# Performance work log

Measured on AMD Instinct MI355X. Metric: run time of the kernel, lower is better.

## Reference

```python
import jax, jax.numpy as jnp
import numpy as np
import math

EPS = 1e-5
K = 4        # conv kernel size
N = 16       # d_state


def setup_inputs() -> dict:
    key = jax.random.key(0)
    b, l, d = 1, 2048, 1024
    di = 2 * d                      # inner channels after split
    dt_rank = math.ceil(d / 16)     # 64
    ks = jax.random.split(key, 8)
    s = 0.02
    return {
        "x": jax.random.normal(ks[0], (b, l, d), jnp.float32),
        "norm_scale": jnp.ones((d,), jnp.float32),
        "w_in": jax.random.normal(ks[1], (d, 4 * d), jnp.float32) * s,
        "conv_w": jax.random.normal(ks[2], (K, 1, di), jnp.float32) * 0.2,
        "conv_b": jnp.zeros((di,), jnp.float32),
        "A_log": jax.random.normal(ks[3], (di, N), jnp.float32) * 0.5,
        "D": jax.random.normal(ks[4], (di,), jnp.float32) * 0.1,
        "w_xproj": jax.random.normal(ks[5], (di, dt_rank + 2 * N), jnp.float32) * s,
        "w_dt": jax.random.normal(ks[6], (dt_rank, di), jnp.float32) * s,
        "b_dt": jnp.zeros((di,), jnp.float32),
        "w_out": jax.random.normal(ks[7], (di, d), jnp.float32) * s,
    }


def _causal_depthwise_conv(x, w, b):
    # x: (b,l,c), w: (K,1,c). Original pads (K-1,K-1) then slices [:, :l] == causal left-pad.
    c = x.shape[-1]
    y = jax.lax.conv_general_dilated(
        x, w, window_strides=(1,), padding=[(K - 1, 0)],
        dimension_numbers=("NWC", "WIO", "NWC"), feature_group_count=c)
    return y + b


def reference(x, norm_scale, w_in, conv_w, conv_b, A_log, D, w_xproj, w_dt, b_dt, w_out):
    dt_rank = w_dt.shape[0]
    # RMSNorm (mean=False, bias=False), scale only
    h = x * jax.lax.rsqrt(jnp.mean(x * x, axis=-1, keepdims=True) + EPS) * norm_scale
    h = h @ w_in                         # (b,l,4d)
    xs, res = jnp.split(h, 2, axis=-1)   # each (b,l,2d)
    res = jax.nn.silu(res)
    xs = jax.nn.silu(_causal_depthwise_conv(xs, conv_w, conv_b))
    proj = xs @ w_xproj                  # (b,l,dt_rank+2N)
    delta, B, C = jnp.split(proj, [dt_rank, dt_rank + N], axis=-1)
    delta = jax.nn.softplus(delta @ w_dt + b_dt)          # (b,l,c)
    A = -jnp.exp(A_log)                                   # (c,n)
    deltaA = jnp.exp(delta[..., None] * A)                # (b,l,c,n)
    deltaBx = (delta * xs)[..., None] * B[:, :, None, :]  # (b,l,c,n)

    def combine(e_i, e_j):
        a_i, b_i = e_i
        a_j, b_j = e_j
        return (a_i * a_j, a_j * b_i + b_j)

    _, ys = jax.lax.associative_scan(combine, (deltaA, deltaBx), axis=1)
    y = jnp.einsum("blcn,bln->blc", ys, C)
    out = (y + xs * D) * res
    return x + out @ w_out
```

## Files before the change

kernel.cpp:

```cpp
#include <hip/hip_runtime.h>

typedef short short8 __attribute__((ext_vector_type(8)));
typedef float floatx4 __attribute__((ext_vector_type(4)));
typedef unsigned int u32;

__device__ __forceinline__ float b2f(unsigned short u) {
    union { unsigned int i; float f; } v; v.i = ((unsigned int)u) << 16; return v.f;
}
__device__ __forceinline__ float hi2f(u32 p) {
    union { unsigned int i; float f; } v; v.i = p & 0xFFFF0000u; return v.f;
}
__device__ __forceinline__ float lo2f(u32 p) {
    union { unsigned int i; float f; } v; v.i = p << 16; return v.f;
}
__device__ __forceinline__ unsigned short f2b(float f) {
    union { unsigned int i; float f; } v; v.f = f;
    unsigned int r = v.i + 0x7FFFu + ((v.i >> 16) & 1u);
    return (unsigned short)(r >> 16);
}
__device__ __forceinline__ float ld(const void* p, size_t i, int f) {
    return f ? ((const float*)p)[i] : b2f(((const unsigned short*)p)[i]);
}
__device__ __forceinline__ void ld4(const void* p, size_t i, int f, float* o) {
    if (f) {
        float4 v = *(const float4*)((const float*)p + i);
        o[0] = v.x; o[1] = v.y; o[2] = v.z; o[3] = v.w;
    } else {
        uint2 v = *(const uint2*)((const unsigned short*)p + i);
        const unsigned short* vp = (const unsigned short*)&v;
        o[0] = b2f(vp[0]); o[1] = b2f(vp[1]); o[2] = b2f(vp[2]); o[3] = b2f(vp[3]);
    }
}
__device__ __forceinline__ int dtf(const void* scale) {
    return (((const unsigned short*)scale)[0] == 0x3F80u) ? 0 : 1;
}
__device__ __forceinline__ void gload16(const unsigned short* g, unsigned short* l) {
    __builtin_amdgcn_global_load_lds(
        (const __attribute__((address_space(1))) u32*)(const void*)g,
        (__attribute__((address_space(3))) u32*)(void*)l, 16, 0, 0);
}
template<int CTRL>
__device__ __forceinline__ float dpp_add(float y) {
    union { float f; int i; } u, r;
    u.f = y;
    r.i = __builtin_amdgcn_update_dpp(0, u.i, CTRL, 0xF, 0xF, true);
    return y + r.f;
}

__global__ __launch_bounds__(256) void prep_kernel(
    const void* x, const void* scale, unsigned short* __restrict__ h,
    const void* w_in, unsigned short* __restrict__ wT,
    const void* w_out, unsigned short* __restrict__ woT)
{
    const int f = dtf(scale);
    const int b = blockIdx.x, tid = threadIdx.x;
    if (b < 2048) {
        const int t = b, i0 = tid * 4;
        float xv[4], sv[4];
        ld4(x, (size_t)t * 1024 + i0, f, xv);
        ld4(scale, (size_t)i0, f, sv);
        float ss = xv[0] * xv[0] + xv[1] * xv[1] + xv[2] * xv[2] + xv[3] * xv[3];
        #pragma unroll
        for (int o = 32; o > 0; o >>= 1) ss += __shfl_down(ss, o);
        __shared__ float sr[4];
        if ((tid & 63) == 0) sr[tid >> 6] = ss;
        __syncthreads();
        float r = rsqrtf((sr[0] + sr[1] + sr[2] + sr[3]) * (1.f / 1024.f) + 1e-5f);
        unsigned short o4[4];
        #pragma unroll
        for (int j = 0; j < 4; j++) o4[j] = f2b(xv[j] * r * sv[j]);
        *(uint2*)(h + (size_t)t * 1024 + i0) = *(const uint2*)o4;
    } else if (b < 3072) {
        __shared__ __align__(8) unsigned short tile[64][72];
        const int idx = b - 2048;
        const int n0 = (idx & 63) * 64, k0 = (idx >> 6) * 64;
        const int r = tid >> 2, cb = (tid & 3) * 16;
        #pragma unroll
        for (int j = 0; j < 4; j++) {
            int c = cb + j * 4;
            float v[4]; unsigned short o4[4];
            ld4(w_in, (size_t)(k0 + r) * 4096 + n0 + c, f, v);
            o4[0] = f2b(v[0]); o4[1] = f2b(v[1]); o4[2] = f2b(v[2]); o4[3] = f2b(v[3]);
            *(uint2*)&tile[r][c] = *(const uint2*)o4;
        }
        __syncthreads();
        #pragma unroll
        for (int j = 0; j < 4; j++) {
            int k = cb + j * 4;
            unsigned short o4[4];
            o4[0] = tile[k][r]; o4[1] = tile[k + 1][r];
            o4[2] = tile[k + 2][r]; o4[3] = tile[k + 3][r];
            *(uint2*)(wT + (size_t)(n0 + r) * 1024 + k0 + k) = *(const uint2*)o4;
        }
    } else {
        __shared__ __align__(8) unsigned short tile[64][72];
        const int idx = b - 3072;
        const int n0 = (idx & 15) * 64, k0 = (idx >> 4) * 64;
        const int r = tid >> 2, cb = (tid & 3) * 16;
        #pragma unroll
        for (int j = 0; j < 4; j++) {
            int c = cb + j * 4;
            float v[4]; unsigned short o4[4];
            ld4(w_out, (size_t)(k0 + r) * 1024 + n0 + c, f, v);
            o4[0] = f2b(v[0]); o4[1] = f2b(v[1]); o4[2] = f2b(v[2]); o4[3] = f2b(v[3]);
            *(uint2*)&tile[r][c] = *(const uint2*)o4;
        }
        __syncthreads();
        #pragma unroll
        for (int j = 0; j < 4; j++) {
            int k = cb + j * 4;
            unsigned short o4[4];
            o4[0] = tile[k][r]; o4[1] = tile[k + 1][r];
            o4[2] = tile[k + 2][r]; o4[3] = tile[k + 3][r];
            *(uint2*)(woT + (size_t)(n0 + r) * 2048 + k0 + k) = *(const uint2*)o4;
        }
    }
}

template<int KDIM, int NDIM, int TM, int TN, int MODE, int XW>
__global__ __launch_bounds__(256) void gemm_bt_kernel(
    const unsigned short* __restrict__ A, const unsigned short* __restrict__ BT,
    void* out0, unsigned short* out1, const void* xres, const void* nscale)
{
    constexpr int RT = TM / 32;
    constexpr int NT = TN / 32;
    constexpr int GX = NDIM / TN, GY = 2048 / TM;
    constexpr int SW = GX / XW, SH = GY / (8 / XW);
    const int f = dtf(nscale);
    __shared__ __align__(16) unsigned short As[TM * 64];
    __shared__ __align__(16) unsigned short Bs[TN * 64];
    const int t = threadIdx.x, w = t >> 6, lane = t & 63;
    const int q = lane >> 4, low = lane & 15;
    const int bid = blockIdx.y * GX + blockIdx.x;
    const int xcd = bid & 7, cc = bid >> 3;
    const int bx = (xcd % XW) * SW + cc % SW;
    const int by = (xcd / XW) * SH + cc / SW;
    const int row0 = by * TM, n0 = bx * TN;
    const int wy = w >> 1, wx = w & 1;

    floatx4 acc[RT][NT];
    #pragma unroll
    for (int i = 0; i < RT; i++)
        #pragma unroll
        for (int j = 0; j < NT; j++) acc[i][j] = (floatx4){0.f, 0.f, 0.f, 0.f};

    const int srow = lane >> 3, scol = (lane & 7) * 8;
    const unsigned short* a_src = A + (size_t)(row0 + w * (TM / 4) + srow) * KDIM + scol;
    const unsigned short* b_src = BT + (size_t)(n0 + w * (TN / 4) + srow) * KDIM + scol;

    for (int k0 = 0; k0 < KDIM; k0 += 64) {
        #pragma unroll
        for (int i = 0; i < TM / 32; i++)
            gload16(a_src + k0 + i * 8 * KDIM, &As[(w * (TM / 4) + i * 8) * 64]);
        #pragma unroll
        for (int i = 0; i < TN / 32; i++)
            gload16(b_src + k0 + i * 8 * KDIM, &Bs[(w * (TN / 4) + i * 8) * 64]);
        __syncthreads();
        #pragma unroll
        for (int kh = 0; kh < 2; kh++) {
            short8 af[RT];
            #pragma unroll
            for (int rt = 0; rt < RT; rt++)
                af[rt] = *(const short8*)&As[(wy * (TM / 2) + rt * 16 + low) * 64 + kh * 32 + q * 8];
            #pragma unroll
            for (int nt = 0; nt < NT; nt++) {
                short8 bf = *(const short8*)&Bs[(wx * (TN / 2) + nt * 16 + low) * 64 + kh * 32 + q * 8];
                #pragma unroll
                for (int rt = 0; rt < RT; rt++)
                    acc[rt][nt] = __builtin_amdgcn_mfma_f32_16x16x32_bf16(af[rt], bf, acc[rt][nt], 0, 0, 0);
            }
        }
        __syncthreads();
    }

    #pragma unroll
    for (int nt = 0; nt < NT; nt++) {
        const int col = n0 + wx * (TN / 2) + nt * 16 + low;
        #pragma unroll
        for (int rt = 0; rt < RT; rt++) {
            #pragma unroll
            for (int r = 0; r < 4; r++) {
                const int row = row0 + wy * (TM / 2) + rt * 16 + q * 4 + r;
                float v = acc[rt][nt][r];
                if (MODE == 0) {
                    if (col < NDIM / 2) {
                        ((unsigned short*)out0)[(size_t)row * (NDIM / 2) + col] = f2b(v);
                    } else {
                        float s = v / (1.f + __expf(-v));
                        out1[(size_t)row * (NDIM / 2) + (col - NDIM / 2)] = f2b(s);
                    }
                } else {
                    size_t idx = (size_t)row * NDIM + col;
                    float o = v + ld(xres, idx, f);
                    if (f) ((float*)out0)[idx] = o;
                    else   ((unsigned short*)out0)[idx] = f2b(o);
                }
            }
        }
    }
}

__global__ __launch_bounds__(256) void conv_kernel(
    const unsigned short* __restrict__ xs_raw, const void* conv_w,
    const void* conv_b, unsigned short* __restrict__ xs_conv, const void* nscale)
{
    const int f = dtf(nscale);
    int id = blockIdx.x * 256 + threadIdx.x;
    int t = id >> 8, c8 = (id & 255) * 8;
    float acc[8];
    if (f) {
        const float* bf = (const float*)conv_b + c8;
        float4 b0 = *(const float4*)bf, b1 = *(const float4*)(bf + 4);
        acc[0] = b0.x; acc[1] = b0.y; acc[2] = b0.z; acc[3] = b0.w;
        acc[4] = b1.x; acc[5] = b1.y; acc[6] = b1.z; acc[7] = b1.w;
    } else {
        uint4 bv = *(const uint4*)((const unsigned short*)conv_b + c8);
        const unsigned short* bp = (const unsigned short*)&bv;
        #pragma unroll
        for (int j = 0; j < 8; j++) acc[j] = b2f(bp[j]);
    }
    #pragma unroll
    for (int k = 0; k < 4; k++) {
        int tt = t - 3 + k;
        if (tt >= 0) {
            uint4 xv = *(const uint4*)(xs_raw + (size_t)tt * 2048 + c8);
            const unsigned short* xp = (const unsigned short*)&xv;
            float wv[8];
            if (f) {
                const float* wf = (const float*)conv_w + (size_t)k * 2048 + c8;
                float4 w0 = *(const float4*)wf, w1 = *(const float4*)(wf + 4);
                wv[0] = w0.x; wv[1] = w0.y; wv[2] = w0.z; wv[3] = w0.w;
                wv[4] = w1.x; wv[5] = w1.y; wv[6] = w1.z; wv[7] = w1.w;
            } else {
                uint4 wu = *(const uint4*)((const unsigned short*)conv_w + (size_t)k * 2048 + c8);
                const unsigned short* wp = (const unsigned short*)&wu;
                #pragma unroll
                for (int j = 0; j < 8; j++) wv[j] = b2f(wp[j]);
            }
            #pragma unroll
            for (int j = 0; j < 8; j++) acc[j] += wv[j] * b2f(xp[j]);
        }
    }
    unsigned short outv[8];
    #pragma unroll
    for (int j = 0; j < 8; j++) {
        float s = acc[j] / (1.f + __expf(-acc[j]));
        outv[j] = f2b(s);
    }
    *(uint4*)(xs_conv + (size_t)t * 2048 + c8) = *(const uint4*)outv;
}

__global__ __launch_bounds__(256) void xproj_gemm_kernel(
    const unsigned short* __restrict__ A, const void* B,
    float* __restrict__ proj, const void* nscale)
{
    const int f = dtf(nscale);
    __shared__ __align__(16) unsigned short As[64 * 32];
    __shared__ __align__(16) unsigned short Bs[64 * 32];
    const int t = threadIdx.x;
    const int row0 = blockIdx.y * 64, n0 = blockIdx.x * 64;
    const int ks = blockIdx.z;
    const int wave = t >> 6, lane = t & 63;
    const int q = lane >> 4, low = lane & 15;
    floatx4 acc[4];
    #pragma unroll
    for (int i = 0; i < 4; i++) acc[i] = (floatx4){0.f, 0.f, 0.f, 0.f};
    const int ar = t >> 2, ac = (t & 3) * 8;
    const int bk = t >> 3, bn = (t & 7) * 8;
    const int col0 = n0 + bn;
    const int kbeg = ks * 256, kend = kbeg + 256;
    for (int k0 = kbeg; k0 < kend; k0 += 32) {
        uint4 av = *(const uint4*)(A + (size_t)(row0 + ar) * 2048 + k0 + ac);
        *(uint4*)&As[ar * 32 + ac] = av;
        unsigned short bu[8];
        if (col0 < 96) {
            if (f) {
                const float* Bf = (const float*)B + (size_t)(k0 + bk) * 96 + col0;
                float4 b0 = *(const float4*)Bf, b1 = *(const float4*)(Bf + 4);
                bu[0] = f2b(b0.x); bu[1] = f2b(b0.y); bu[2] = f2b(b0.z); bu[3] = f2b(b0.w);
                bu[4] = f2b(b1.x); bu[5] = f2b(b1.y); bu[6] = f2b(b1.z); bu[7] = f2b(b1.w);
            } else {
                uint4 bv = *(const uint4*)((const unsigned short*)B + (size_t)(k0 + bk) * 96 + col0);
                *(uint4*)bu = bv;
            }
        } else {
            #pragma unroll
            for (int j = 0; j < 8; j++) bu[j] = 0;
        }
        #pragma unroll
        for (int j = 0; j < 8; j++) Bs[(bn + j) * 32 + bk] = bu[j];
        __syncthreads();
        short8 af = *(const short8*)&As[(wave * 16 + low) * 32 + q * 8];
        #pragma unroll
        for (int i = 0; i < 4; i++) {
            short8 bfr = *(const short8*)&Bs[(i * 16 + low) * 32 + q * 8];
            acc[i] = __builtin_amdgcn_mfma_f32_16x16x32_bf16(af, bfr, acc[i], 0, 0, 0);
        }
        __syncthreads();
    }
    #pragma unroll
    for (int i = 0; i < 4; i++) {
        int col = n0 + i * 16 + low;
        if (col < 96) {
            #pragma unroll
            for (int r = 0; r < 4; r++) {
                int row = row0 + wave * 16 + q * 4 + r;
                atomicAdd(&proj[(size_t)row * 128 + col], acc[i][r]);
            }
        }
    }
}

__global__ __launch_bounds__(256) void delta_gemm_kernel(
    const float* __restrict__ proj, const void* B, const void* b_dt,
    unsigned short* __restrict__ delta, const void* nscale)
{
    const int f = dtf(nscale);
    __shared__ __align__(16) unsigned short As[64 * 32];
    __shared__ __align__(16) unsigned short Bs[64 * 32];
    const int t = threadIdx.x;
    const int row0 = blockIdx.y * 64, n0 = blockIdx.x * 64;
    const int wave = t >> 6, lane = t & 63;
    const int q = lane >> 4, low = lane & 15;
    floatx4 acc[4];
    #pragma unroll
    for (int i = 0; i < 4; i++) acc[i] = (floatx4){0.f, 0.f, 0.f, 0.f};
    const int ar = t >> 2, ac = (t & 3) * 8;
    const int bk = t >> 3, bn = (t & 7) * 8;
    #pragma unroll
    for (int k0 = 0; k0 < 64; k0 += 32) {
        const float* Ap = proj + (size_t)(row0 + ar) * 128 + k0 + ac;
        float4 a0 = *(const float4*)Ap, a1 = *(const float4*)(Ap + 4);
        As[ar * 32 + ac + 0] = f2b(a0.x); As[ar * 32 + ac + 1] = f2b(a0.y);
        As[ar * 32 + ac + 2] = f2b(a0.z); As[ar * 32 + ac + 3] = f2b(a0.w);
        As[ar * 32 + ac + 4] = f2b(a1.x); As[ar * 32 + ac + 5] = f2b(a1.y);
        As[ar * 32 + ac + 6] = f2b(a1.z); As[ar * 32 + ac + 7] = f2b(a1.w);
        unsigned short bu[8];
        if (f) {
            const float* Bp = (const float*)B + (size_t)(k0 + bk) * 2048 + n0 + bn;
            float4 b0 = *(const float4*)Bp, b1 = *(const float4*)(Bp + 4);
            bu[0] = f2b(b0.x); bu[1] = f2b(b0.y); bu[2] = f2b(b0.z); bu[3] = f2b(b0.w);
            bu[4] = f2b(b1.x); bu[5] = f2b(b1.y); bu[6] = f2b(b1.z); bu[7] = f2b(b1.w);
        } else {
            uint4 bv = *(const uint4*)((const unsigned short*)B + (size_t)(k0 + bk) * 2048 + n0 + bn);
            const unsigned short* bp = (const unsigned short*)&bv;
            #pragma unroll
            for (int j = 0; j < 8; j++) bu[j] = bp[j];
        }
        #pragma unroll
        for (int j = 0; j < 8; j++) Bs[(bn + j) * 32 + bk] = bu[j];
        __syncthreads();
        short8 af = *(const short8*)&As[(wave * 16 + low) * 32 + q * 8];
        #pragma unroll
        for (int i = 0; i < 4; i++) {
            short8 bfr = *(const short8*)&Bs[(i * 16 + low) * 32 + q * 8];
            acc[i] = __builtin_amdgcn_mfma_f32_16x16x32_bf16(af, bfr, acc[i], 0, 0, 0);
        }
        __syncthreads();
    }
    #pragma unroll
    for (int i = 0; i < 4; i++) {
        int col = n0 + i * 16 + low;
        float bias = ld(b_dt, col, f);
        #pragma unroll
        for (int r = 0; r < 4; r++) {
            int row = row0 + wave * 16 + q * 4 + r;
            float v = acc[i][r] + bias;
            float sp = fmaxf(v, 0.f) + log1pf(__expf(-fabsf(v)));
            delta[(size_t)row * 2048 + col] = f2b(sp);
        }
    }
}

__global__ __launch_bounds__(256, 8) void scanA_kernel(
    const unsigned short* __restrict__ delta, const unsigned short* __restrict__ xs,
    const float* __restrict__ proj, const void* A_log,
    float2* __restrict__ AS, const void* nscale)
{
    const int f = dtf(nscale);
    const int chunk = blockIdx.x, c0 = blockIdx.y * 16, t0 = chunk * 64;
    __shared__ __align__(16) float2 dvx[16 * 68];
    __shared__ __align__(16) float Bt[16 * 68];
    const int tid = threadIdx.x;
    #pragma unroll
    for (int j = 0; j < 2; j++) {
        int idx = tid + 256 * j;
        int t = idx >> 3, cp = (idx & 7) * 2;
        u32 dpair = *(const u32*)(delta + (size_t)(t0 + t) * 2048 + c0 + cp);
        u32 xpair = *(const u32*)(xs    + (size_t)(t0 + t) * 2048 + c0 + cp);
        float dv0 = lo2f(dpair), dv1 = hi2f(dpair);
        float xv0 = lo2f(xpair), xv1 = hi2f(xpair);
        dvx[cp * 68 + t]       = make_float2(dv0, dv0 * xv0);
        dvx[(cp + 1) * 68 + t] = make_float2(dv1, dv1 * xv1);
    }
    #pragma unroll
    for (int j = 0; j < 4; j++) {
        int idx = tid + 256 * j;
        int t = idx >> 4, n = idx & 15;
        Bt[n * 68 + t] = proj[(size_t)(t0 + t) * 128 + 64 + n];
    }
    __syncthreads();
    const int cl = tid >> 4, n = tid & 15;
    const float A = -__expf(ld(A_log, (size_t)(c0 + cl) * 16 + n, f)) * 1.4426950408889634f;
    float sl = 0.f, sdv = 0.f;
    for (int t4 = 0; t4 < 64; t4 += 4) {
        float4 q0 = *(const float4*)&dvx[cl * 68 + t4];
        float4 q1 = *(const float4*)&dvx[cl * 68 + t4 + 2];
        float4 b4 = *(const float4*)&Bt[n * 68 + t4];
        float a0 = __builtin_amdgcn_exp2f(q0.x * A);
        sl = a0 * sl + q0.y * b4.x; sdv += q0.x;
        float a1 = __builtin_amdgcn_exp2f(q0.z * A);
        sl = a1 * sl + q0.w * b4.y; sdv += q0.z;
        float a2 = __builtin_amdgcn_exp2f(q1.x * A);
        sl = a2 * sl + q1.y * b4.z; sdv += q1.x;
        float a3 = __builtin_amdgcn_exp2f(q1.z * A);
        sl = a3 * sl + q1.w * b4.w; sdv += q1.z;
    }
    float ap = __builtin_amdgcn_exp2f(A * sdv);
    AS[(size_t)chunk * 32768 + (size_t)c0 * 16 + tid] = make_float2(ap, sl);
}

__global__ __launch_bounds__(256, 8) void scanC_kernel(
    const unsigned short* __restrict__ delta, const unsigned short* __restrict__ xs,
    const float* __restrict__ proj, const void* A_log, const void* Dv,
    const float2* __restrict__ AS,
    const unsigned short* __restrict__ res, unsigned short* __restrict__ inner,
    const void* nscale)
{
    const int f = dtf(nscale);
    const int chunk = blockIdx.x, c0 = blockIdx.y * 16, t0 = chunk * 64;
    __shared__ __align__(16) float2 dvx[16 * 68];
    __shared__ __align__(16) float Bt[16 * 68];
    __shared__ __align__(16) float Ct[16 * 68];
    __shared__ __align__(16) float yl[16 * 68];
    __shared__ __align__(16) float xD[16 * 68];
    const int tid = threadIdx.x;
    const int g = c0 * 16 + tid;
    float pred = 0.f;
    for (int k = 0; k < chunk; k += 8) {
        float2 v0, v1, v2, v3, v4, v5, v6, v7;
        if (k + 0 < chunk) v0 = AS[(size_t)(k + 0) * 32768 + g];
        if (k + 1 < chunk) v1 = AS[(size_t)(k + 1) * 32768 + g];
        if (k + 2 < chunk) v2 = AS[(size_t)(k + 2) * 32768 + g];
        if (k + 3 < chunk) v3 = AS[(size_t)(k + 3) * 32768 + g];
        if (k + 4 < chunk) v4 = AS[(size_t)(k + 4) * 32768 + g];
        if (k + 5 < chunk) v5 = AS[(size_t)(k + 5) * 32768 + g];
        if (k + 6 < chunk) v6 = AS[(size_t)(k + 6) * 32768 + g];
        if (k + 7 < chunk) v7 = AS[(size_t)(k + 7) * 32768 + g];
        if (k + 0 < chunk) pred = v0.x * pred + v0.y;
        if (k + 1 < chunk) pred = v1.x * pred + v1.y;
        if (k + 2 < chunk) pred = v2.x * pred + v2.y;
        if (k + 3 < chunk) pred = v3.x * pred + v3.y;
        if (k + 4 < chunk) pred = v4.x * pred + v4.y;
        if (k + 5 < chunk) pred = v5.x * pred + v5.y;
        if (k + 6 < chunk) pred = v6.x * pred + v6.y;
        if (k + 7 < chunk) pred = v7.x * pred + v7.y;
    }
    #pragma unroll
    for (int j = 0; j < 2; j++) {
        int idx = tid + 256 * j;
        int t = idx >> 3, cp = (idx & 7) * 2;
        u32 dpair = *(const u32*)(delta + (size_t)(t0 + t) * 2048 + c0 + cp);
        u32 xpair = *(const u32*)(xs    + (size_t)(t0 + t) * 2048 + c0 + cp);
        float dv0 = lo2f(dpair), dv1 = hi2f(dpair);
        float xv0 = lo2f(xpair), xv1 = hi2f(xpair);
        float D0 = ld(Dv, c0 + cp, f), D1 = ld(Dv, c0 + cp + 1, f);
        dvx[cp * 68 + t]       = make_float2(dv0, dv0 * xv0);
        dvx[(cp + 1) * 68 + t] = make_float2(dv1, dv1 * xv1);
        xD[cp * 68 + t]        = xv0 * D0;
        xD[(cp + 1) * 68 + t]  = xv1 * D1;
    }
    #pragma unroll
    for (int j = 0; j < 4; j++) {
        int idx = tid + 256 * j;
        int t = idx >> 4, n = idx & 15;
        Bt[n * 68 + t] = proj[(size_t)(t0 + t) * 128 + 64 + n];
        Ct[n * 68 + t] = proj[(size_t)(t0 + t) * 128 + 80 + n];
    }
    __syncthreads();
    const int cl = tid >> 4, n = tid & 15;
    const float A = -__expf(ld(A_log, (size_t)(c0 + cl) * 16 + n, f)) * 1.4426950408889634f;
    float s = pred;
    for (int t4 = 0; t4 < 64; t4 += 4) {
        float4 q0 = *(const float4*)&dvx[cl * 68 + t4];
        float4 q1 = *(const float4*)&dvx[cl * 68 + t4 + 2];
        float4 b4 = *(const float4*)&Bt[n * 68 + t4];
        float4 c4 = *(const float4*)&Ct[n * 68 + t4];
        float dvv[4] = {q0.x, q0.z, q1.x, q1.z};
        float uv[4]  = {q0.y, q0.w, q1.y, q1.w};
        const float* bp = (const float*)&b4;
        const float* cp = (const float*)&c4;
        #pragma unroll
        for (int j = 0; j < 4; j++) {
            float a = __builtin_amdgcn_exp2f(dvv[j] * A);
            s = a * s + uv[j] * bp[j];
            float y = s * cp[j];
            y = dpp_add<0x111>(y);
            y = dpp_add<0x112>(y);
            y = dpp_add<0x114>(y);
            y = dpp_add<0x118>(y);
            if (n == 15) yl[cl * 68 + t4 + j] = y;
        }
    }
    __syncthreads();
    const int et = tid >> 2, ech = (tid & 3) * 4;
    size_t gbase = (size_t)(t0 + et) * 2048 + c0 + ech;
    uint2 rv2 = *(const uint2*)(res + gbase);
    const unsigned short* rp = (const unsigned short*)&rv2;
    unsigned short outv[4];
    #pragma unroll
    for (int j = 0; j < 4; j++) {
        int c = ech + j;
        float o = (yl[c * 68 + et] + xD[c * 68 + et]) * b2f(rp[j]);
        outv[j] = f2b(o);
    }
    *(uint2*)(inner + gbase) = *(const uint2*)outv;
}

extern "C" void kernel_launch(void* const* d_in, const int* in_sizes, int n_in,
                              void* d_out, int out_size, void* d_ws, size_t ws_size,
                              hipStream_t stream) {
    const void* x       = d_in[0];
    const void* nscale  = d_in[1];
    const void* w_in    = d_in[2];
    const void* conv_w  = d_in[3];
    const void* conv_b  = d_in[4];
    const void* A_log   = d_in[5];
    const void* Dv      = d_in[6];
    const void* w_xproj = d_in[7];
    const void* w_dt    = d_in[8];
    const void* b_dt    = d_in[9];
    const void* w_out   = d_in[10];

    char* ws = (char*)d_ws;
    const size_t MB = 1048576;
    unsigned short* xs_raw  = (unsigned short*)(ws);
    unsigned short* res_s   = (unsigned short*)(ws + 8 * MB);
    unsigned short* xs_conv = (unsigned short*)(ws + 16 * MB);
    unsigned short* delta   = (unsigned short*)(ws + 24 * MB);
    unsigned short* h_norm  = (unsigned short*)(ws + 32 * MB);
    unsigned short* wT      = (unsigned short*)(ws + 36 * MB);
    unsigned short* woT     = (unsigned short*)(ws + 44 * MB);
    float*          proj    = (float*)(ws + 56 * MB);
    float2*         AS      = (float2*)(ws + 57 * MB);
    unsigned short* inner   = res_s;

    hipMemsetAsync(proj, 0, 2048 * 128 * sizeof(float), stream);

    prep_kernel<<<3584, 256, 0, stream>>>(x, nscale, h_norm, w_in, wT, w_out, woT);
    gemm_bt_kernel<1024, 4096, 128, 64, 0, 8><<<dim3(64, 16), 256, 0, stream>>>(
        h_norm, wT, xs_raw, res_s, nullptr, nscale);
    conv_kernel<<<2048, 256, 0, stream>>>(xs_raw, conv_w, conv_b, xs_conv, nscale);
    xproj_gemm_kernel<<<dim3(2, 32, 8), 256, 0, stream>>>(xs_conv, w_xproj, proj, nscale);
    delta_gemm_kernel<<<dim3(32, 32), 256, 0, stream>>>(proj, w_dt, b_dt, delta, nscale);
    scanA_kernel<<<dim3(32, 128), 256, 0, stream>>>(delta, xs_conv, proj, A_log, AS, nscale);
    scanC_kernel<<<dim3(32, 128), 256, 0, stream>>>(delta, xs_conv, proj, A_log, Dv, AS, res_s, inner, nscale);
    gemm_bt_kernel<2048, 1024, 64, 64, 1, 2><<<dim3(16, 32), 256, 0, stream>>>(
        inner, woT, d_out, nullptr, x, nscale);
}
```

Baseline: 251.3 us.

## Fuse delta projection GEMM and softplus into both scan kernels

Removes the separate delta_gemm kernel and its bf16 delta buffer. Each scan block now recomputes its own 64x16 delta tile with a small MFMA over the 64-wide dt rank, applies bias and softplus, and keeps the result in shared memory. This saves one launch and the global write plus two reads of a 2048x2048 array. In exchange the delta GEMM runs twice (once in scanA, once in scanC), each block re-reads proj rows and w_dt columns, and shared memory per block grows with the launch-bound occupancy hint of 8 dropped.

```diff
diff --git a/kernel.cpp b/kernel.cpp
--- a/kernel.cpp
+++ b/kernel.cpp
@@ -311,93 +311,73 @@
     }
 }
 
-__global__ __launch_bounds__(256) void delta_gemm_kernel(
-    const float* __restrict__ proj, const void* B, const void* b_dt,
-    unsigned short* __restrict__ delta, const void* nscale)
-{
-    const int f = dtf(nscale);
-    __shared__ __align__(16) unsigned short As[64 * 32];
-    __shared__ __align__(16) unsigned short Bs[64 * 32];
-    const int t = threadIdx.x;
-    const int row0 = blockIdx.y * 64, n0 = blockIdx.x * 64;
-    const int wave = t >> 6, lane = t & 63;
-    const int q = lane >> 4, low = lane & 15;
-    floatx4 acc[4];
-    #pragma unroll
-    for (int i = 0; i < 4; i++) acc[i] = (floatx4){0.f, 0.f, 0.f, 0.f};
-    const int ar = t >> 2, ac = (t & 3) * 8;
-    const int bk = t >> 3, bn = (t & 7) * 8;
-    #pragma unroll
-    for (int k0 = 0; k0 < 64; k0 += 32) {
-        const float* Ap = proj + (size_t)(row0 + ar) * 128 + k0 + ac;
-        float4 a0 = *(const float4*)Ap, a1 = *(const float4*)(Ap + 4);
-        As[ar * 32 + ac + 0] = f2b(a0.x); As[ar * 32 + ac + 1] = f2b(a0.y);
-        As[ar * 32 + ac + 2] = f2b(a0.z); As[ar * 32 + ac + 3] = f2b(a0.w);
-        As[ar * 32 + ac + 4] = f2b(a1.x); As[ar * 32 + ac + 5] = f2b(a1.y);
-        As[ar * 32 + ac + 6] = f2b(a1.z); As[ar * 32 + ac + 7] = f2b(a1.w);
-        unsigned short bu[8];
-        if (f) {
-            const float* Bp = (const float*)B + (size_t)(k0 + bk) * 2048 + n0 + bn;
-            float4 b0 = *(const float4*)Bp, b1 = *(const float4*)(Bp + 4);
-            bu[0] = f2b(b0.x); bu[1] = f2b(b0.y); bu[2] = f2b(b0.z); bu[3] = f2b(b0.w);
-            bu[4] = f2b(b1.x); bu[5] = f2b(b1.y); bu[6] = f2b(b1.z); bu[7] = f2b(b1.w);
-        } else {
-            uint4 bv = *(const uint4*)((const unsigned short*)B + (size_t)(k0 + bk) * 2048 + n0 + bn);
-            const unsigned short* bp = (const unsigned short*)&bv;
-            #pragma unroll
-            for (int j = 0; j < 8; j++) bu[j] = bp[j];
-        }
-        #pragma unroll
-        for (int j = 0; j < 8; j++) Bs[(bn + j) * 32 + bk] = bu[j];
-        __syncthreads();
-        short8 af = *(const short8*)&As[(wave * 16 + low) * 32 + q * 8];
-        #pragma unroll
-        for (int i = 0; i < 4; i++) {
-            short8 bfr = *(const short8*)&Bs[(i * 16 + low) * 32 + q * 8];
-            acc[i] = __builtin_amdgcn_mfma_f32_16x16x32_bf16(af, bfr, acc[i], 0, 0, 0);
-        }
-        __syncthreads();
-    }
-    #pragma unroll
-    for (int i = 0; i < 4; i++) {
-        int col = n0 + i * 16 + low;
-        float bias = ld(b_dt, col, f);
-        #pragma unroll
-        for (int r = 0; r < 4; r++) {
-            int row = row0 + wave * 16 + q * 4 + r;
-            float v = acc[i][r] + bias;
-            float sp = fmaxf(v, 0.f) + log1pf(__expf(-fabsf(v)));
-            delta[(size_t)row * 2048 + col] = f2b(sp);
-        }
-    }
-}
-
-__global__ __launch_bounds__(256, 8) void scanA_kernel(
-    const unsigned short* __restrict__ delta, const unsigned short* __restrict__ xs,
-    const float* __restrict__ proj, const void* A_log,
+__global__ __launch_bounds__(256) void scanA_kernel(
+    const unsigned short* __restrict__ xs, const float* __restrict__ proj,
+    const void* w_dt, const void* b_dt, const void* A_log,
     float2* __restrict__ AS, const void* nscale)
 {
     const int f = dtf(nscale);
     const int chunk = blockIdx.x, c0 = blockIdx.y * 16, t0 = chunk * 64;
+    __shared__ __align__(16) float  xl [16 * 68];
     __shared__ __align__(16) float2 dvx[16 * 68];
-    __shared__ __align__(16) float Bt[16 * 68];
+    __shared__ __align__(16) float  Bt [16 * 68];
+    __shared__ __align__(16) char   ovl[64 * 72 * 2 + 16 * 72 * 2];
+    __shared__ float bl[16];
+    unsigned short* Asd = (unsigned short*)ovl;
+    unsigned short* Bsd = (unsigned short*)(ovl + 64 * 72 * 2);
     const int tid = threadIdx.x;
     #pragma unroll
     for (int j = 0; j < 2; j++) {
         int idx = tid + 256 * j;
         int t = idx >> 3, cp = (idx & 7) * 2;
-        u32 dpair = *(const u32*)(delta + (size_t)(t0 + t) * 2048 + c0 + cp);
-        u32 xpair = *(const u32*)(xs    + (size_t)(t0 + t) * 2048 + c0 + cp);
-        float dv0 = lo2f(dpair), dv1 = hi2f(dpair);
-        float xv0 = lo2f(xpair), xv1 = hi2f(xpair);
-        dvx[cp * 68 + t]       = make_float2(dv0, dv0 * xv0);
-        dvx[(cp + 1) * 68 + t] = make_float2(dv1, dv1 * xv1);
-    }
+        u32 xpair = *(const u32*)(xs + (size_t)(t0 + t) * 2048 + c0 + cp);
+        xl[cp * 68 + t]       = lo2f(xpair);
+        xl[(cp + 1) * 68 + t] = hi2f(xpair);
+    }
+    {
+        const int ar = tid >> 2, ac = (tid & 3) * 16;
+        #pragma unroll
+        for (int j = 0; j < 4; j++) {
+            float4 a = *(const float4*)(proj + (size_t)(t0 + ar) * 128 + ac + j * 4);
+            unsigned short o4[4] = {f2b(a.x), f2b(a.y), f2b(a.z), f2b(a.w)};
+            *(uint2*)&Asd[ar * 72 + ac + j * 4] = *(const uint2*)o4;
+        }
+    }
+    {
+        const int k = tid >> 2, c4 = (tid & 3) * 4;
+        #pragma unroll
+        for (int j = 0; j < 4; j++) {
+            int c = c4 + j;
+            Bsd[c * 72 + k] = f2b(ld(w_dt, (size_t)k * 2048 + c0 + c, f));
+        }
+    }
+    if (tid < 16) bl[tid] = ld(b_dt, c0 + tid, f);
     #pragma unroll
     for (int j = 0; j < 4; j++) {
         int idx = tid + 256 * j;
         int t = idx >> 4, n = idx & 15;
         Bt[n * 68 + t] = proj[(size_t)(t0 + t) * 128 + 64 + n];
+    }
+    __syncthreads();
+    {
+        const int w = tid >> 6, lane = tid & 63;
+        const int q = lane >> 4, low = lane & 15;
+        floatx4 dacc = (floatx4){0.f, 0.f, 0.f, 0.f};
+        #pragma unroll
+        for (int kh = 0; kh < 2; kh++) {
+            short8 af = *(const short8*)&Asd[(w * 16 + low) * 72 + kh * 32 + q * 8];
+            short8 bf = *(const short8*)&Bsd[low * 72 + kh * 32 + q * 8];
+            dacc = __builtin_amdgcn_mfma_f32_16x16x32_bf16(af, bf, dacc, 0, 0, 0);
+        }
+        float bias = bl[low];
+        #pragma unroll
+        for (int r = 0; r < 4; r++) {
+            float v = dacc[r] + bias;
+            float sp = fmaxf(v, 0.f) + log1pf(__expf(-fabsf(v)));
+            int tl = w * 16 + q * 4 + r;
+            float xv = xl[low * 68 + tl];
+            dvx[low * 68 + tl] = make_float2(sp, sp * xv);
+        }
     }
     __syncthreads();
     const int cl = tid >> 4, n = tid & 15;
@@ -420,20 +400,25 @@
     AS[(size_t)chunk * 32768 + (size_t)c0 * 16 + tid] = make_float2(ap, sl);
 }
 
-__global__ __launch_bounds__(256, 8) void scanC_kernel(
-    const unsigned short* __restrict__ delta, const unsigned short* __restrict__ xs,
-    const float* __restrict__ proj, const void* A_log, const void* Dv,
+__global__ __launch_bounds__(256) void scanC_kernel(
+    const unsigned short* __restrict__ xs, const float* __restrict__ proj,
+    const void* w_dt, const void* b_dt, const void* A_log, const void* Dv,
     const float2* __restrict__ AS,
     const unsigned short* __restrict__ res, unsigned short* __restrict__ inner,
     const void* nscale)
 {
     const int f = dtf(nscale);
     const int chunk = blockIdx.x, c0 = blockIdx.y * 16, t0 = chunk * 64;
+    __shared__ __align__(16) float  xl [16 * 68];
     __shared__ __align__(16) float2 dvx[16 * 68];
-    __shared__ __align__(16) float Bt[16 * 68];
-    __shared__ __align__(16) float Ct[16 * 68];
-    __shared__ __align__(16) float yl[16 * 68];
-    __shared__ __align__(16) float xD[16 * 68];
+    __shared__ __align__(16) float  Bt [16 * 68];
+    __shared__ __align__(16) char   ovl[64 * 72 * 2 + 16 * 72 * 2];
+    __shared__ float bl[16];
+    __shared__ float Dl[16];
+    unsigned short* Asd = (unsigned short*)ovl;
+    unsigned short* Bsd = (unsigned short*)(ovl + 64 * 72 * 2);
+    float* Ct = (float*)ovl;
+    float* yl = (float*)(ovl + 16 * 68 * 4);
     const int tid = threadIdx.x;
     const int g = c0 * 16 + tid;
     float pred = 0.f;
@@ -460,21 +445,60 @@
     for (int j = 0; j < 2; j++) {
         int idx = tid + 256 * j;
         int t = idx >> 3, cp = (idx & 7) * 2;
-        u32 dpair = *(const u32*)(delta + (size_t)(t0 + t) * 2048 + c0 + cp);
-        u32 xpair = *(const u32*)(xs    + (size_t)(t0 + t) * 2048 + c0 + cp);
-        float dv0 = lo2f(dpair), dv1 = hi2f(dpair);
-        float xv0 = lo2f(xpair), xv1 = hi2f(xpair);
-        float D0 = ld(Dv, c0 + cp, f), D1 = ld(Dv, c0 + cp + 1, f);
-        dvx[cp * 68 + t]       = make_float2(dv0, dv0 * xv0);
-        dvx[(cp + 1) * 68 + t] = make_float2(dv1, dv1 * xv1);
-        xD[cp * 68 + t]        = xv0 * D0;
-        xD[(cp + 1) * 68 + t]  = xv1 * D1;
-    }
+        u32 xpair = *(const u32*)(xs + (size_t)(t0 + t) * 2048 + c0 + cp);
+        xl[cp * 68 + t]       = lo2f(xpair);
+        xl[(cp + 1) * 68 + t] = hi2f(xpair);
+    }
+    {
+        const int ar = tid >> 2, ac = (tid & 3) * 16;
+        #pragma unroll
+        for (int j = 0; j < 4; j++) {
+            float4 a = *(const float4*)(proj + (size_t)(t0 + ar) * 128 + ac + j * 4);
+            unsigned short o4[4] = {f2b(a.x), f2b(a.y), f2b(a.z), f2b(a.w)};
+            *(uint2*)&Asd[ar * 72 + ac + j * 4] = *(const uint2*)o4;
+        }
+    }
+    {
+        const int k = tid >> 2, c4 = (tid & 3) * 4;
+        #pragma unroll
+        for (int j = 0; j < 4; j++) {
+            int c = c4 + j;
+            Bsd[c * 72 + k] = f2b(ld(w_dt, (size_t)k * 2048 + c0 + c, f));
+        }
+    }
+    if (tid < 16) { bl[tid] = ld(b_dt, c0 + tid, f); Dl[tid] = ld(Dv, c0 + tid, f); }
     #pragma unroll
     for (int j = 0; j < 4; j++) {
         int idx = tid + 256 * j;
         int t = idx >> 4, n = idx & 15;
         Bt[n * 68 + t] = proj[(size_t)(t0 + t) * 128 + 64 + n];
+    }
+    __syncthreads();
+    {
+        const int w = tid >> 6, lane = tid & 63;
+        const int q = lane >> 4, low = lane & 15;
+        floatx4 dacc = (floatx4){0.f, 0.f, 0.f, 0.f};
+        #pragma unroll
+        for (int kh = 0; kh < 2; kh++) {
+            short8 af = *(const short8*)&Asd[(w * 16 + low) * 72 + kh * 32 + q * 8];
+            short8 bf = *(const short8*)&Bsd[low * 72 + kh * 32 + q * 8];
+            dacc = __builtin_amdgcn_mfma_f32_16x16x32_bf16(af, bf, dacc, 0, 0, 0);
+        }
+        float bias = bl[low];
+        #pragma unroll
+        for (int r = 0; r < 4; r++) {
+            float v = dacc[r] + bias;
+            float sp = fmaxf(v, 0.f) + log1pf(__expf(-fabsf(v)));
+            int tl = w * 16 + q * 4 + r;
+            float xv = xl[low * 68 + tl];
+            dvx[low * 68 + tl] = make_float2(sp, sp * xv);
+        }
+    }
+    __syncthreads();
+    #pragma unroll
+    for (int j = 0; j < 4; j++) {
+        int idx = tid + 256 * j;
+        int t = idx >> 4, n = idx & 15;
         Ct[n * 68 + t] = proj[(size_t)(t0 + t) * 128 + 80 + n];
     }
     __syncthreads();
@@ -511,7 +535,7 @@
     #pragma unroll
     for (int j = 0; j < 4; j++) {
         int c = ech + j;
-        float o = (yl[c * 68 + et] + xD[c * 68 + et]) * b2f(rp[j]);
+        float o = (yl[c * 68 + et] + xl[c * 68 + et] * Dl[c]) * b2f(rp[j]);
         outv[j] = f2b(o);
     }
     *(uint2*)(inner + gbase) = *(const uint2*)outv;
@@ -537,7 +561,6 @@
     unsigned short* xs_raw  = (unsigned short*)(ws);
     unsigned short* res_s   = (unsigned short*)(ws + 8 * MB);
     unsigned short* xs_conv = (unsigned short*)(ws + 16 * MB);
-    unsigned short* delta   = (unsigned short*)(ws + 24 * MB);
     unsigned short* h_norm  = (unsigned short*)(ws + 32 * MB);
     unsigned short* wT      = (unsigned short*)(ws + 36 * MB);
     unsigned short* woT     = (unsigned short*)(ws + 44 * MB);
@@ -552,9 +575,10 @@
         h_norm, wT, xs_raw, res_s, nullptr, nscale);
     conv_kernel<<<2048, 256, 0, stream>>>(xs_raw, conv_w, conv_b, xs_conv, nscale);
     xproj_gemm_kernel<<<dim3(2, 32, 8), 256, 0, stream>>>(xs_conv, w_xproj, proj, nscale);
-    delta_gemm_kernel<<<dim3(32, 32), 256, 0, stream>>>(proj, w_dt, b_dt, delta, nscale);
-    scanA_kernel<<<dim3(32, 128), 256, 0, stream>>>(delta, xs_conv, proj, A_log, AS, nscale);
-    scanC_kernel<<<dim3(32, 128), 256, 0, stream>>>(delta, xs_conv, proj, A_log, Dv, AS, res_s, inner, nscale);
+    scanA_kernel<<<dim3(32, 128), 256, 0, stream>>>(
+        xs_conv, proj, w_dt, b_dt, A_log, AS, nscale);
+    scanC_kernel<<<dim3(32, 128), 256, 0, stream>>>(
+        xs_conv, proj, w_dt, b_dt, A_log, Dv, AS, res_s, inner, nscale);
     gemm_bt_kernel<2048, 1024, 64, 64, 1, 2><<<dim3(16, 32), 256, 0, stream>>>(
         inner, woT, d_out, nullptr, x, nscale);
 }
```

Result: slower. 266.1 us (+5.9%).
